# Optimization experiments

Hardware: AMD Instinct MI355X
Metric: run time of the kernel (lower is better)

Reference implementation:

```python
import jax, jax.numpy as jnp
import numpy as np

HIDDEN = 2560
NH = 32            # num_attention_heads
HD = HIDDEN // NH  # head_size = 80
RD = 32            # rotary_dim = int(0.4 * 80)
THETA = 10000.0
B, S = 2, 2048


def _rope_cos_sin(position_ids):
    # neox-style partial RoPE over the first RD dims of each head
    inv_freq = 1.0 / (THETA ** (jnp.arange(0, RD, 2, dtype=jnp.float32) / RD))  # [RD/2]
    freqs = position_ids.astype(jnp.float32)[..., None] * inv_freq  # [B,S,RD/2]
    return jnp.cos(freqs), jnp.sin(freqs)


def _apply_rope(x, cos, sin):
    # x: [B,S,NH,HD]; rotate first RD dims (neox: halves are paired)
    rot, rest = x[..., :RD], x[..., RD:]
    x1, x2 = rot[..., : RD // 2], rot[..., RD // 2:]
    c = cos[:, :, None, :]
    s = sin[:, :, None, :]
    o1 = x1 * c - x2 * s
    o2 = x2 * c + x1 * s
    return jnp.concatenate([o1, o2, rest], axis=-1)


def setup_inputs() -> dict:
    key = jax.random.key(0)
    ks = jax.random.split(key, 6)
    position_ids = jnp.tile(jnp.arange(S, dtype=jnp.int64)[None, :], (B, 1))
    return {
        "position_ids": position_ids,
        "hidden_states": jax.random.normal(ks[0], (B, S, HIDDEN), dtype=jnp.float32),
        "w_qkv": jax.random.normal(ks[1], (HIDDEN, 3 * HIDDEN), dtype=jnp.float32) * 0.02,
        "b_qkv": jax.random.normal(ks[2], (3 * HIDDEN,), dtype=jnp.float32) * 0.02,
        "w_dense": jax.random.normal(ks[3], (HIDDEN, HIDDEN), dtype=jnp.float32) * 0.02,
        "b_dense": jax.random.normal(ks[4], (HIDDEN,), dtype=jnp.float32) * 0.02,
    }


def reference(position_ids, hidden_states, w_qkv, b_qkv, w_dense, b_dense):
    scale = HD ** -0.5
    qkv = hidden_states @ w_qkv + b_qkv          # [B,S,3*HIDDEN]
    q, k, v = jnp.split(qkv, 3, axis=-1)
    q = q.reshape(B, S, NH, HD)
    k = k.reshape(B, S, NH, HD)
    v = v.reshape(B, S, NH, HD)
    cos, sin = _rope_cos_sin(position_ids)
    q = _apply_rope(q, cos, sin)
    k = _apply_rope(k, cos, sin)
    scores = jnp.einsum("bqhd,bkhd->bhqk", q, k) * scale  # [B,NH,S,S]
    causal = jnp.tril(jnp.ones((S, S), dtype=bool))
    scores = jnp.where(causal[None, None], scores, jnp.finfo(scores.dtype).min)
    probs = jax.nn.softmax(scores, axis=-1)
    attn = jnp.einsum("bhqk,bkhd->bqhd", probs, v).reshape(B, S, HIDDEN)
    return attn @ w_dense + b_dense
```

## Files before the change

kernel.cpp:

```cpp
#include <hip/hip_runtime.h>

#define S_LEN 2048
#define NHEAD 32
#define HD 80
#define DPAD 96
#define HIDDEN 2560
#define QKV_N 7680

typedef __attribute__((ext_vector_type(8))) short bf16x8;
typedef __attribute__((ext_vector_type(8))) unsigned short u16x8;
typedef __attribute__((ext_vector_type(4))) float f32x4;

__device__ __forceinline__ unsigned short f2bf(float f) {
  unsigned int u = __float_as_uint(f);
  u += 0x7fffu + ((u >> 16) & 1u);
  return (unsigned short)(u >> 16);
}
__device__ __forceinline__ float bf2f(unsigned short h) {
  return __uint_as_float(((unsigned int)h) << 16);
}

__device__ __forceinline__ void gload16(const void* g, void* l) {
  __builtin_amdgcn_global_load_lds((const __attribute__((address_space(1))) void*)g,
                                   (__attribute__((address_space(3))) void*)l, 16, 0, 0);
}

__global__ __launch_bounds__(256) void k_cvt(const float* __restrict__ in,
                                             unsigned short* __restrict__ out, int n4) {
  int i = blockIdx.x * 256 + threadIdx.x;
  if (i >= n4) return;
  float4 v = reinterpret_cast<const float4*>(in)[i];
  ushort4 o;
  o.x = f2bf(v.x); o.y = f2bf(v.y); o.z = f2bf(v.z); o.w = f2bf(v.w);
  reinterpret_cast<ushort4*>(out)[i] = o;
}

__global__ __launch_bounds__(256) void k_transpose_bf16(const float* __restrict__ in,
                                                        unsigned short* __restrict__ out,
                                                        int R, int C) {
  __shared__ float tile[64][68];
  int tc = blockIdx.x * 64, tr = blockIdx.y * 64;
  for (int i = threadIdx.x; i < 64 * 16; i += 256) {
    int r = i >> 4, c4 = i & 15;
    float4 v = *(const float4*)&in[(size_t)(tr + r) * C + tc + c4 * 4];
    *(float4*)&tile[r][c4 * 4] = v;
  }
  __syncthreads();
  for (int i = threadIdx.x; i < 8 * 64; i += 256) {
    int ro = i >> 6, c = i & 63;
    u16x8 v;
#pragma unroll
    for (int j = 0; j < 8; ++j) v[j] = f2bf(tile[ro * 8 + j][c]);
    *(u16x8*)&out[(size_t)(tc + c) * R + tr + ro * 8] = v;
  }
}

__global__ __launch_bounds__(512, 2)
void k_gemm_qkv(const unsigned short* __restrict__ A,
                const unsigned short* __restrict__ Bt,
                const float* __restrict__ bias,
                unsigned short* __restrict__ Cbf,
                int M, int N, int K) {
  __shared__ unsigned short sA[4][8192];
  __shared__ unsigned short sB[4][8192];
  const int nbm = M >> 8, nbn = N >> 8;
  const int CM = nbm >> 2, CN = nbn >> 1;
  {
  }
  int wg = blockIdx.x;
  const int xcd = wg & 7;
  const int idx = wg >> 3;
  const int bm = (xcd >> 1) * CM + idx / CN;
  const int bn = (xcd & 1) * CN + idx % CN;
  const int tid = threadIdx.x;
  const int lane = tid & 63, wave = tid >> 6;
  const int wr = wave >> 2, wc = wave & 3;
  const int lc = lane & 15, lr = lane >> 4;

  const int sub = (lane & 7) ^ (lane >> 3);
  const int rstage = wave * 16 + ((lane >> 3) << 1) + (sub >> 2);
  const int cstage = (sub & 3) * 8;
  const unsigned short* Agp = A + (size_t)(bm * 256 + rstage) * K + cstage;
  const unsigned short* Bgp = Bt + (size_t)(bn * 256 + rstage) * K + cstage;
  const size_t halfoff = (size_t)128 * K;

  const int loff = ((lc >> 1) << 7) + (((((lc & 1) << 2) | lr) ^ (lc >> 1)) << 4);

  f32x4 acc[8][4];
  const f32x4 zero = {0.f, 0.f, 0.f, 0.f};
#pragma unroll
  for (int m = 0; m < 8; ++m)
#pragma unroll
    for (int n = 0; n < 4; ++n) acc[m][n] = zero;

  auto stage = [&](int buf, int t) {
    gload16(Agp + t * 32, &sA[buf][wave * 512]);
    gload16(Agp + halfoff + t * 32, &sA[buf][4096 + wave * 512]);
    gload16(Bgp + t * 32, &sB[buf][wave * 512]);
    gload16(Bgp + halfoff + t * 32, &sB[buf][4096 + wave * 512]);
  };

  const int NT = K >> 5;
#pragma unroll
  for (int t = 0; t < 3; ++t) stage(t, t);

  const int nj = NT >> 2;
  for (int j = 0; j < nj; ++j) {
#pragma unroll
    for (int to = 0; to < 4; ++to) {
      const int t = (j << 2) + to;
      if (t < NT - 2)       asm volatile("s_waitcnt vmcnt(8)" ::: "memory");
      else if (t == NT - 2) asm volatile("s_waitcnt vmcnt(4)" ::: "memory");
      else                  asm volatile("s_waitcnt vmcnt(0)" ::: "memory");
      __builtin_amdgcn_s_barrier();
      asm volatile("" ::: "memory");

      const char* bufA = (const char*)&sA[to][0];
      const char* bufB = (const char*)&sB[to][0];
      bf16x8 af[8], bfr[4];
#pragma unroll
      for (int mi = 0; mi < 8; ++mi)
        af[mi] = *(const bf16x8*)(bufA + ((wr * 128 + mi * 16) << 6) + loff);
#pragma unroll
      for (int ni = 0; ni < 4; ++ni)
        bfr[ni] = *(const bf16x8*)(bufB + ((wc * 64 + ni * 16) << 6) + loff);

      if (t + 3 < NT) stage((to + 3) & 3, t + 3);

      asm volatile("s_waitcnt lgkmcnt(0)" ::: "memory");
      __builtin_amdgcn_sched_barrier(0);
      __builtin_amdgcn_s_setprio(1);
#pragma unroll
      for (int mi = 0; mi < 8; ++mi)
#pragma unroll
        for (int ni = 0; ni < 4; ++ni)
          acc[mi][ni] = __builtin_amdgcn_mfma_f32_16x16x32_bf16(af[mi], bfr[ni], acc[mi][ni], 0, 0, 0);
      __builtin_amdgcn_s_setprio(0);
    }
  }

  const int rowb = bm * 256 + wr * 128;
  const int colb = bn * 256 + wc * 64;
#pragma unroll
  for (int ni = 0; ni < 4; ++ni) {
    const int col = colb + ni * 16 + lc;
    const float bv = bias[col];
#pragma unroll
    for (int mf = 0; mf < 8; ++mf) {
#pragma unroll
      for (int jj = 0; jj < 4; ++jj) {
        const int row = rowb + mf * 16 + lr * 4 + jj;
        Cbf[(size_t)row * N + col] = f2bf(acc[mf][ni][jj] + bv);
      }
    }
  }
}

__global__ __launch_bounds__(256, 3)
void k_gemm_out(const unsigned short* __restrict__ A,
                const unsigned short* __restrict__ Bt,
                const float* __restrict__ bias,
                float* __restrict__ Cf,
                int M, int N, int K) {
  __shared__ unsigned short sA[3][4096];
  __shared__ unsigned short sB[3][4096];
  const int nbm = M >> 7, nbn = N >> 7;
  const int CM = nbm >> 2, CN = nbn >> 1;
  int wg = blockIdx.x;
  const int xcd = wg & 7;
  const int idx = wg >> 3;
  const int bm = (xcd >> 1) * CM + idx / CN;
  const int bn = (xcd & 1) * CN + idx % CN;
  const int tid = threadIdx.x;
  const int lane = tid & 63, wave = tid >> 6;
  const int wr = wave >> 1, wc = wave & 1;
  const int lc = lane & 15, lr = lane >> 4;

  const int sub = (lane & 7) ^ (lane >> 3);
  const int rstage = wave * 16 + ((lane >> 3) << 1) + (sub >> 2);
  const int cstage = (sub & 3) * 8;
  const unsigned short* Agp = A + (size_t)(bm * 128 + rstage) * K + cstage;
  const unsigned short* Bgp = Bt + (size_t)(bn * 128 + rstage) * K + cstage;
  const size_t halfoff = (size_t)64 * K;

  const int loff = ((lc >> 1) << 7) + (((((lc & 1) << 2) | lr) ^ (lc >> 1)) << 4);

  f32x4 acc[4][4];
  const f32x4 zero = {0.f, 0.f, 0.f, 0.f};
#pragma unroll
  for (int m = 0; m < 4; ++m)
#pragma unroll
    for (int n = 0; n < 4; ++n) acc[m][n] = zero;

  auto stage = [&](int buf, int t) {
    gload16(Agp + t * 32, &sA[buf][wave * 512]);
    gload16(Agp + halfoff + t * 32, &sA[buf][2048 + wave * 512]);
    gload16(Bgp + t * 32, &sB[buf][wave * 512]);
    gload16(Bgp + halfoff + t * 32, &sB[buf][2048 + wave * 512]);
  };

  const int NT = K >> 5;
  stage(0, 0);
  stage(1, 1);
  int b0 = 0;
  for (int t = 0; t < NT; ++t) {
    if (t < NT - 1) asm volatile("s_waitcnt vmcnt(4)" ::: "memory");
    else            asm volatile("s_waitcnt vmcnt(0)" ::: "memory");
    __builtin_amdgcn_s_barrier();
    asm volatile("" ::: "memory");

    const char* bufA = (const char*)&sA[b0][0];
    const char* bufB = (const char*)&sB[b0][0];
    bf16x8 af[4], bfr[4];
#pragma unroll
    for (int mi = 0; mi < 4; ++mi)
      af[mi] = *(const bf16x8*)(bufA + ((wr * 64 + mi * 16) << 6) + loff);
#pragma unroll
    for (int ni = 0; ni < 4; ++ni)
      bfr[ni] = *(const bf16x8*)(bufB + ((wc * 64 + ni * 16) << 6) + loff);

    if (t + 2 < NT) {
      int bs = b0 - 1; if (bs < 0) bs = 2;
      stage(bs, t + 2);
    }

    asm volatile("s_waitcnt lgkmcnt(0)" ::: "memory");
    __builtin_amdgcn_sched_barrier(0);
    __builtin_amdgcn_s_setprio(1);
#pragma unroll
    for (int mi = 0; mi < 4; ++mi)
#pragma unroll
      for (int ni = 0; ni < 4; ++ni)
        acc[mi][ni] = __builtin_amdgcn_mfma_f32_16x16x32_bf16(af[mi], bfr[ni], acc[mi][ni], 0, 0, 0);
    __builtin_amdgcn_s_setprio(0);
    ++b0; if (b0 == 3) b0 = 0;
  }

  const int rowb = bm * 128 + wr * 64;
  const int colb = bn * 128 + wc * 64;
#pragma unroll
  for (int ni = 0; ni < 4; ++ni) {
    const int col = colb + ni * 16 + lc;
    const float bv = bias[col];
#pragma unroll
    for (int mf = 0; mf < 4; ++mf) {
#pragma unroll
      for (int jj = 0; jj < 4; ++jj) {
        const int row = rowb + mf * 16 + lr * 4 + jj;
        Cf[(size_t)row * N + col] = acc[mf][ni][jj] + bv;
      }
    }
  }
}

__global__ __launch_bounds__(256) void k_rope(const unsigned short* __restrict__ qkv,
                                              unsigned short* __restrict__ Qw,
                                              unsigned short* __restrict__ Kw,
                                              unsigned short* __restrict__ Vt) {
  const int blk = blockIdx.x;
  const int sc = blk & 31;
  const int bh = blk >> 5;
  const int b = bh >> 5, h = bh & 31;
  const int s0 = sc * 64;
  __shared__ float cs0[64][16], sn0[64][16];
  __shared__ unsigned short vbuf[64][88];
  const int tid = threadIdx.x;
  for (int i = tid; i < 64 * 16; i += 256) {
    int sl = i >> 4, fi = i & 15;
    float ang = (float)(s0 + sl) * __expf(-(float)fi * 0.575646273248511421f);
    cs0[sl][fi] = cosf(ang);
    sn0[sl][fi] = sinf(ang);
  }
  const size_t row0 = (size_t)(b * S_LEN + s0) * QKV_N;
  for (int i = tid; i < 64 * 10; i += 256) {
    int sl = i / 10, o = i - sl * 10;
    *(u16x8*)&vbuf[sl][o * 8] =
        *(const u16x8*)&qkv[row0 + (size_t)sl * QKV_N + 2 * HIDDEN + h * HD + o * 8];
  }
  __syncthreads();
  const size_t obase = ((size_t)bh * S_LEN + s0) * DPAD;
  const float SCALE = 0.111803398874989485f;
  for (int i = tid; i < 64 * 12; i += 256) {
    int sl = i / 12, o = i - sl * 12;
    u16x8 outq = {0, 0, 0, 0, 0, 0, 0, 0};
    u16x8 outk = {0, 0, 0, 0, 0, 0, 0, 0};
    if (o < 10) {
      const unsigned short* rp = qkv + row0 + (size_t)sl * QKV_N + h * HD;
      u16x8 xq = *(const u16x8*)(rp + o * 8);
      u16x8 xk = *(const u16x8*)(rp + HIDDEN + o * 8);
      if (o < 2) {
        u16x8 yq = *(const u16x8*)(rp + (o + 2) * 8);
        u16x8 yk = *(const u16x8*)(rp + HIDDEN + (o + 2) * 8);
#pragma unroll
        for (int j = 0; j < 8; ++j) {
          float c = cs0[sl][o * 8 + j], s = sn0[sl][o * 8 + j];
          outq[j] = f2bf((bf2f(xq[j]) * c - bf2f(yq[j]) * s) * SCALE);
          outk[j] = f2bf(bf2f(xk[j]) * c - bf2f(yk[j]) * s);
        }
      } else if (o < 4) {
        u16x8 yq = *(const u16x8*)(rp + (o - 2) * 8);
        u16x8 yk = *(const u16x8*)(rp + HIDDEN + (o - 2) * 8);
#pragma unroll
        for (int j = 0; j < 8; ++j) {
          float c = cs0[sl][(o - 2) * 8 + j], s = sn0[sl][(o - 2) * 8 + j];
          outq[j] = f2bf((bf2f(xq[j]) * c + bf2f(yq[j]) * s) * SCALE);
          outk[j] = f2bf(bf2f(xk[j]) * c + bf2f(yk[j]) * s);
        }
      } else {
#pragma unroll
        for (int j = 0; j < 8; ++j) {
          outq[j] = f2bf(bf2f(xq[j]) * SCALE);
          outk[j] = xk[j];
        }
      }
    }
    *(u16x8*)&Qw[obase + (size_t)sl * DPAD + o * 8] = outq;
    *(u16x8*)&Kw[obase + (size_t)sl * DPAD + o * 8] = outk;
  }
  const size_t vtb = (size_t)bh * DPAD * S_LEN + s0;
  for (int i = tid; i < 80 * 8; i += 256) {
    int d = i >> 3, so = i & 7;
    u16x8 v;
#pragma unroll
    for (int j = 0; j < 8; ++j) v[j] = vbuf[so * 8 + j][d];
    *(u16x8*)&Vt[vtb + (size_t)d * S_LEN + so * 8] = v;
  }
}

__global__ __launch_bounds__(256, 2) void k_attn(const unsigned short* __restrict__ Qw,
                                                 const unsigned short* __restrict__ Kw,
                                                 const unsigned short* __restrict__ Vt,
                                                 unsigned short* __restrict__ O) {
  __shared__ unsigned short sK[2][64 * 104];
  __shared__ unsigned short sV[2][80 * 72];
  __shared__ unsigned short sP[4][16 * 72];
  const int p = blockIdx.x;
  const int bh = blockIdx.y;
  const int b = bh >> 5, h = bh & 31;
  const int tid = threadIdx.x;
  const int wave = tid >> 6, lane = tid & 63;
  const int lr = lane >> 4, lc = lane & 15;
  unsigned short* Pw = &sP[wave][0];

  const unsigned short* Kh = Kw + (size_t)bh * S_LEN * DPAD;
  const unsigned short* Vh = Vt + (size_t)bh * DPAD * S_LEN;
  const unsigned short* Qh = Qw + (size_t)bh * S_LEN * DPAD;

  const int kr = tid >> 2, kc = (tid & 3) * 24;
  const int vr = tid >> 3, vc = (tid & 7) * 8;

  u16x8 kst0, kst1, kst2, vst0, vst1, vst2;
  auto gload = [&](int t) {
    const unsigned short* Kg = Kh + ((size_t)(t * 64 + kr)) * DPAD + kc;
    kst0 = *(const u16x8*)(Kg);
    kst1 = *(const u16x8*)(Kg + 8);
    kst2 = *(const u16x8*)(Kg + 16);
    const unsigned short* Vg = Vh + (size_t)vr * S_LEN + t * 64 + vc;
    vst0 = *(const u16x8*)(Vg);
    vst1 = *(const u16x8*)(Vg + 32 * S_LEN);
    if (tid < 128) vst2 = *(const u16x8*)(Vg + (size_t)64 * S_LEN);
  };
  auto swrite = [&](int buf) {
    *(u16x8*)&sK[buf][kr * 104 + kc] = kst0;
    *(u16x8*)&sK[buf][kr * 104 + kc + 8] = kst1;
    *(u16x8*)&sK[buf][kr * 104 + kc + 16] = kst2;
    *(u16x8*)&sV[buf][vr * 72 + vc] = vst0;
    *(u16x8*)&sV[buf][(vr + 32) * 72 + vc] = vst1;
    if (tid < 128) *(u16x8*)&sV[buf][(vr + 64) * 72 + vc] = vst2;
  };

  const f32x4 zero = {0.f, 0.f, 0.f, 0.f};

#pragma unroll 1
  for (int qi = 0; qi < 2; ++qi) {
    const int qt = qi ? (15 - p) : p;
    const int nt = 2 * qt + 2;
    const int wbase = qt * 128 + wave * 32;

    bf16x8 qf[2][3];
#pragma unroll
    for (int m = 0; m < 2; ++m)
#pragma unroll
      for (int ks = 0; ks < 3; ++ks)
        qf[m][ks] = *(const bf16x8*)&Qh[(size_t)(wbase + m * 16 + lc) * DPAD + ks * 32 + lr * 8];

    f32x4 oacc[2][5];
#pragma unroll
    for (int m = 0; m < 2; ++m)
#pragma unroll
      for (int n = 0; n < 5; ++n) oacc[m][n] = zero;
    float mrun[2] = {-1e30f, -1e30f}, lrun[2] = {0.f, 0.f};

    gload(0);
    __syncthreads();
    swrite(0);
    int cur = 0;

#pragma unroll 1
    for (int t = 0; t < nt; ++t) {
      __syncthreads();
      if (t + 1 < nt) gload(t + 1);
      const int ktb = t * 64;
      const bool act0 = ktb <= wbase + 15;
      const bool act1 = ktb <= wbase + 31;
      if (act1) {
        const unsigned short* Kc = sK[cur];
        const unsigned short* Vc = sV[cur];
        f32x4 sf[2][4];
#pragma unroll
        for (int n = 0; n < 4; ++n) {
          sf[0][n] = zero; sf[1][n] = zero;
#pragma unroll
          for (int ks = 0; ks < 3; ++ks) {
            bf16x8 kf = *(const bf16x8*)&Kc[(n * 16 + lc) * 104 + ks * 32 + lr * 8];
            if (act0) sf[0][n] = __builtin_amdgcn_mfma_f32_16x16x32_bf16(kf, qf[0][ks], sf[0][n], 0, 0, 0);
            sf[1][n] = __builtin_amdgcn_mfma_f32_16x16x32_bf16(kf, qf[1][ks], sf[1][n], 0, 0, 0);
          }
        }
        bf16x8 vf[5][2];
#pragma unroll
        for (int n = 0; n < 5; ++n)
#pragma unroll
          for (int ks = 0; ks < 2; ++ks)
            vf[n][ks] = *(const bf16x8*)&Vc[(n * 16 + lc) * 72 + ks * 32 + lr * 8];
#pragma unroll
        for (int m = 0; m < 2; ++m) {
          if (m == 0 && !act0) continue;
          const int qrow0 = wbase + m * 16;
          if (ktb + 63 > qrow0) {
#pragma unroll
            for (int n = 0; n < 4; ++n)
#pragma unroll
              for (int j = 0; j < 4; ++j)
                if (ktb + n * 16 + lr * 4 + j > qrow0 + lc) sf[m][n][j] = -1e30f;
          }
          float t0 = sf[m][0][0];
#pragma unroll
          for (int n = 0; n < 4; ++n)
#pragma unroll
            for (int j = 0; j < 4; ++j) t0 = fmaxf(t0, sf[m][n][j]);
          t0 = fmaxf(t0, __shfl_xor(t0, 16));
          t0 = fmaxf(t0, __shfl_xor(t0, 32));
          const float nm = fmaxf(mrun[m], t0);
          const float corrq = __expf(mrun[m] - nm);
          mrun[m] = nm;
          float ps = 0.f;
#pragma unroll
          for (int n = 0; n < 4; ++n)
#pragma unroll
            for (int j = 0; j < 4; ++j) {
              float e = __expf(sf[m][n][j] - nm);
              sf[m][n][j] = e;
              ps += e;
            }
          ps += __shfl_xor(ps, 16);
          ps += __shfl_xor(ps, 32);
          lrun[m] = lrun[m] * corrq + ps;
          float cj[4];
#pragma unroll
          for (int j = 0; j < 4; ++j) cj[j] = __shfl(corrq, lr * 4 + j, 16);
#pragma unroll
          for (int n = 0; n < 5; ++n)
#pragma unroll
            for (int j = 0; j < 4; ++j) oacc[m][n][j] *= cj[j];
#pragma unroll
          for (int n = 0; n < 4; ++n) {
            unsigned lo = (unsigned)f2bf(sf[m][n][0]) | ((unsigned)f2bf(sf[m][n][1]) << 16);
            unsigned hi = (unsigned)f2bf(sf[m][n][2]) | ((unsigned)f2bf(sf[m][n][3]) << 16);
            uint2 u; u.x = lo; u.y = hi;
            *(uint2*)&Pw[lc * 72 + n * 16 + lr * 4] = u;
          }
          asm volatile("" ::: "memory");
          bf16x8 pa0 = *(const bf16x8*)&Pw[lc * 72 + lr * 8];
          bf16x8 pa1 = *(const bf16x8*)&Pw[lc * 72 + 32 + lr * 8];
#pragma unroll
          for (int n = 0; n < 5; ++n) {
            oacc[m][n] = __builtin_amdgcn_mfma_f32_16x16x32_bf16(pa0, vf[n][0], oacc[m][n], 0, 0, 0);
            oacc[m][n] = __builtin_amdgcn_mfma_f32_16x16x32_bf16(pa1, vf[n][1], oacc[m][n], 0, 0, 0);
          }
          asm volatile("" ::: "memory");
        }
      }
      if (t + 1 < nt) swrite(cur ^ 1);
      cur ^= 1;
    }

#pragma unroll
    for (int m = 0; m < 2; ++m) {
      float linv[4];
#pragma unroll
      for (int j = 0; j < 4; ++j) {
        float lj = __shfl(lrun[m], lr * 4 + j, 16);
        linv[j] = 1.f / lj;
      }
      const int q0 = wbase + m * 16 + lr * 4;
#pragma unroll
      for (int n = 0; n < 5; ++n) {
        const int d = n * 16 + lc;
#pragma unroll
        for (int j = 0; j < 4; ++j)
          O[((size_t)(b * S_LEN) + q0 + j) * HIDDEN + h * HD + d] = f2bf(oacc[m][n][j] * linv[j]);
      }
    }
  }
}

extern "C" void kernel_launch(void* const* d_in, const int* in_sizes, int n_in,
                              void* d_out, int out_size, void* d_ws, size_t ws_size,
                              hipStream_t stream) {
  (void)in_sizes; (void)n_in; (void)out_size; (void)ws_size;
  const float* hidden  = (const float*)d_in[1];
  const float* w_qkv   = (const float*)d_in[2];
  const float* b_qkv   = (const float*)d_in[3];
  const float* w_dense = (const float*)d_in[4];
  const float* b_dense = (const float*)d_in[5];
  char* ws = (char*)d_ws;
  unsigned short* Abf   = (unsigned short*)(ws + 0);
  unsigned short* Wqkvt = (unsigned short*)(ws + 20971520);
  unsigned short* Wdt   = (unsigned short*)(ws + 60293120);
  unsigned short* QKVb  = (unsigned short*)(ws + 73400320);
  unsigned short* Qw    = (unsigned short*)(ws + 136314880);
  unsigned short* Kw    = (unsigned short*)(ws + 161480704);
  unsigned short* Vt    = (unsigned short*)(ws + 186646528);
  unsigned short* Obf   = (unsigned short*)(ws + 211812352);

  k_cvt<<<10240, 256, 0, stream>>>(hidden, Abf, 2621440);
  k_transpose_bf16<<<dim3(120, 40), 256, 0, stream>>>(w_qkv, Wqkvt, 2560, 7680);
  k_transpose_bf16<<<dim3(40, 40), 256, 0, stream>>>(w_dense, Wdt, 2560, 2560);
  k_gemm_qkv<<<480, 512, 0, stream>>>(Abf, Wqkvt, b_qkv, QKVb, 4096, 7680, 2560);
  k_rope<<<2048, 256, 0, stream>>>(QKVb, Qw, Kw, Vt);
  k_attn<<<dim3(8, 64), 256, 0, stream>>>(Qw, Kw, Vt, Obf);
  k_gemm_out<<<640, 256, 0, stream>>>(Obf, Wdt, b_dense, (float*)d_out, 4096, 2560, 2560);
}
```

Before: 410.5 us.

## Stage QKV GEMM output through LDS, lazily rescale softmax, flatten attention grid

The QKV GEMM epilogue now writes the biased bf16 results into shared memory per wave and then stores them to global memory as 16-byte vectors, replacing scattered 2-byte stores. The attention kernel skips the running-max update and accumulator rescale unless some row's max grows by more than 8, which saves exp calls and multiplies at the cost of slightly larger intermediate exponent values. The attention launch becomes a flat 1D grid with heads varying fastest, which changes the order in which blocks are scheduled.

```diff
diff --git a/kernel.cpp b/kernel.cpp
--- a/kernel.cpp
+++ b/kernel.cpp
@@ -65,8 +65,6 @@
   __shared__ unsigned short sB[4][8192];
   const int nbm = M >> 8, nbn = N >> 8;
   const int CM = nbm >> 2, CN = nbn >> 1;
-  {
-  }
   int wg = blockIdx.x;
   const int xcd = wg & 7;
   const int idx = wg >> 3;
@@ -139,20 +137,25 @@
     }
   }
 
+  __builtin_amdgcn_s_barrier();
   const int rowb = bm * 256 + wr * 128;
   const int colb = bn * 256 + wc * 64;
+  unsigned short* myl = (wave < 4) ? &sA[wave][0] : &sB[wave - 4][0];
 #pragma unroll
   for (int ni = 0; ni < 4; ++ni) {
-    const int col = colb + ni * 16 + lc;
-    const float bv = bias[col];
-#pragma unroll
-    for (int mf = 0; mf < 8; ++mf) {
-#pragma unroll
-      for (int jj = 0; jj < 4; ++jj) {
-        const int row = rowb + mf * 16 + lr * 4 + jj;
-        Cbf[(size_t)row * N + col] = f2bf(acc[mf][ni][jj] + bv);
-      }
-    }
+    const float bv = bias[colb + ni * 16 + lc];
+#pragma unroll
+    for (int mf = 0; mf < 8; ++mf)
+#pragma unroll
+      for (int jj = 0; jj < 4; ++jj)
+        myl[(mf * 16 + lr * 4 + jj) * 64 + ni * 16 + lc] = f2bf(acc[mf][ni][jj] + bv);
+  }
+  asm volatile("" ::: "memory");
+#pragma unroll
+  for (int i = 0; i < 16; ++i) {
+    const int idx2 = i * 64 + lane;
+    const int r = idx2 >> 3, c = idx2 & 7;
+    *(u16x8*)&Cbf[(size_t)(rowb + r) * N + colb + c * 8] = *(const u16x8*)&myl[r * 64 + c * 8];
   }
 }
 
@@ -334,8 +337,8 @@
   __shared__ unsigned short sK[2][64 * 104];
   __shared__ unsigned short sV[2][80 * 72];
   __shared__ unsigned short sP[4][16 * 72];
-  const int p = blockIdx.x;
-  const int bh = blockIdx.y;
+  const int p = blockIdx.x >> 6;
+  const int bh = blockIdx.x & 63;
   const int b = bh >> 5, h = bh & 31;
   const int tid = threadIdx.x;
   const int wave = tid >> 6, lane = tid & 63;
@@ -441,9 +444,8 @@
             for (int j = 0; j < 4; ++j) t0 = fmaxf(t0, sf[m][n][j]);
           t0 = fmaxf(t0, __shfl_xor(t0, 16));
           t0 = fmaxf(t0, __shfl_xor(t0, 32));
-          const float nm = fmaxf(mrun[m], t0);
-          const float corrq = __expf(mrun[m] - nm);
-          mrun[m] = nm;
+          const bool need = __any(t0 > mrun[m] + 8.f);
+          const float nm = need ? fmaxf(mrun[m], t0) : mrun[m];
           float ps = 0.f;
 #pragma unroll
           for (int n = 0; n < 4; ++n)
@@ -455,14 +457,20 @@
             }
           ps += __shfl_xor(ps, 16);
           ps += __shfl_xor(ps, 32);
-          lrun[m] = lrun[m] * corrq + ps;
-          float cj[4];
-#pragma unroll
-          for (int j = 0; j < 4; ++j) cj[j] = __shfl(corrq, lr * 4 + j, 16);
-#pragma unroll
-          for (int n = 0; n < 5; ++n)
-#pragma unroll
-            for (int j = 0; j < 4; ++j) oacc[m][n][j] *= cj[j];
+          if (need) {
+            const float corrq = __expf(mrun[m] - nm);
+            mrun[m] = nm;
+            lrun[m] = lrun[m] * corrq + ps;
+            float cj[4];
+#pragma unroll
+            for (int j = 0; j < 4; ++j) cj[j] = __shfl(corrq, lr * 4 + j, 16);
+#pragma unroll
+            for (int n = 0; n < 5; ++n)
+#pragma unroll
+              for (int j = 0; j < 4; ++j) oacc[m][n][j] *= cj[j];
+          } else {
+            lrun[m] += ps;
+          }
 #pragma unroll
           for (int n = 0; n < 4; ++n) {
             unsigned lo = (unsigned)f2bf(sf[m][n][0]) | ((unsigned)f2bf(sf[m][n][1]) << 16);
@@ -529,6 +537,6 @@
   k_transpose_bf16<<<dim3(40, 40), 256, 0, stream>>>(w_dense, Wdt, 2560, 2560);
   k_gemm_qkv<<<480, 512, 0, stream>>>(Abf, Wqkvt, b_qkv, QKVb, 4096, 7680, 2560);
   k_rope<<<2048, 256, 0, stream>>>(QKVb, Qw, Kw, Vt);
-  k_attn<<<dim3(8, 64), 256, 0, stream>>>(Qw, Kw, Vt, Obf);
+  k_attn<<<512, 256, 0, stream>>>(Qw, Kw, Vt, Obf);
   k_gemm_out<<<640, 256, 0, stream>>>(Obf, Wdt, b_dense, (float*)d_out, 4096, 2560, 2560);
 }
```

New measurement: 403.2 us. About the same (-1.8%).
